# Kernel optimization log

Measured on AMD Instinct MI355X. Metric: run time of the kernel, lower is better.

Reference implementation:

```python
import jax, jax.numpy as jnp
import numpy as np

B, H, S, D = 2, 16, 2048, 128

def setup_inputs() -> dict:
    key = jax.random.key(0)
    kq, kk, kv = jax.random.split(key, 3)
    Q = jax.random.normal(kq, (B, H, S, D), dtype=jnp.float32)
    K = jax.random.normal(kk, (B, H, S, D), dtype=jnp.float32)
    V = jax.random.normal(kv, (B, H, S, D), dtype=jnp.float32)
    mask = jnp.tril(jnp.ones((S, S), dtype=bool))  # causal: 1 = keep
    return {"Q": Q, "K": K, "V": V, "mask": mask}

def reference(Q, K, V, mask):
    d_k = Q.shape[-1]
    scale = 1.0 / jnp.sqrt(jnp.asarray(d_k, dtype=Q.dtype))
    # [B,H,S,S] scores, matching the naive materialized implementation's math
    scores = jnp.einsum('bhqd,bhkd->bhqk', Q, K) * scale
    scores = jnp.where(mask, scores, jnp.asarray(-1e9, dtype=scores.dtype))
    attn = jax.nn.softmax(scores, axis=-1)
    return jnp.einsum('bhqk,bhkd->bhqd', attn, V)
```

## Files before the change

kernel.cpp:

```cpp
#include <hip/hip_runtime.h>
#include <hip/hip_bf16.h>
#include <stdint.h>

typedef __attribute__((ext_vector_type(8)))  __bf16 bf16x8;
typedef __attribute__((ext_vector_type(16))) float  f32x16;

#define B_  2
#define H_  16
#define S_  2048
#define D_  128
#define BH_ (B_*H_)

__device__ __forceinline__ uint32_t f2bf1(float f){
  uint32_t u = __builtin_bit_cast(uint32_t, f);
  return (u + 0x7fffu + ((u >> 16) & 1u)) >> 16;
}
__device__ __forceinline__ uint32_t pk2(float a, float b){
  return f2bf1(a) | (f2bf1(b) << 16);
}
__device__ __forceinline__ float bf2f(unsigned short u){
  return __builtin_bit_cast(float, (uint32_t)u << 16);
}

__device__ __forceinline__ void gld16(const void* g, void* l){
  __builtin_amdgcn_global_load_lds(
      (const __attribute__((address_space(1))) void*)g,
      (__attribute__((address_space(3))) void*)(uintptr_t)l, 16, 0, 0);
}

__device__ const unsigned char SPLIT_TAB[24] = {
  15*4+1,15*4+2, 7*4+0, 14*4+1,14*4+2, 13*4+1,13*4+2, 6*4+0,
  12*4+1,12*4+2, 11*4+1,11*4+2, 5*4+0, 10*4+1,10*4+2, 9*4+1,9*4+2,
  4*4+0, 8*4+1,8*4+2, 3*4+0, 2*4+0, 1*4+0, 0*4+0
};

__global__ void prep(const float* __restrict__ K, const float* __restrict__ V,
                     unsigned short* __restrict__ Kb, unsigned short* __restrict__ Vt){
  __shared__ __attribute__((aligned(16))) unsigned short t[64*68];
  const int kv0 = blockIdx.x * 64, d0 = blockIdx.y * 64, bh = blockIdx.z;
  const int tid = threadIdx.x;
  const float* Vp = V + (size_t)bh * S_ * D_;
  const float* Kp = K + (size_t)bh * S_ * D_;
  unsigned short* Ko = Kb + (size_t)bh * S_ * D_;
  for (int i = 0; i < 4; i++){
    int f = tid + i*256;
    int kv = f >> 4, c4 = f & 15;
    size_t idx = (size_t)(kv0+kv)*D_ + d0 + c4*4;
    float4 k = *(const float4*)(Kp + idx);
    *(uint2*)(Ko + idx) = make_uint2(pk2(k.x,k.y), pk2(k.z,k.w));
  }
  for (int i = 0; i < 4; i++){
    int f = tid + i*256;
    int kv = f >> 4, c4 = f & 15;
    float4 v = *(const float4*)(Vp + (size_t)(kv0+kv)*D_ + d0 + c4*4);
    *(uint2*)&t[kv*68 + c4*4] = make_uint2(pk2(v.x,v.y), pk2(v.z,v.w));
  }
  __syncthreads();
  unsigned short* Vo = Vt + (size_t)bh * D_ * S_;
  for (int i = 0; i < 4; i++){
    int g = tid + i*256;
    int d = g >> 4, c = g & 15, kv = c*4;
    ushort4 o;
    o.x = t[(kv+0)*68 + d];
    o.y = t[(kv+1)*68 + d];
    o.z = t[(kv+2)*68 + d];
    o.w = t[(kv+3)*68 + d];
    *(ushort4*)(Vo + (size_t)(d0+d)*S_ + kv0 + kv) = o;
  }
}

__global__ __launch_bounds__(256, 2)
void attn_fwd(const float* __restrict__ Q, const unsigned short* __restrict__ Kb,
              const unsigned short* __restrict__ Vt, float* __restrict__ Out,
              unsigned short* __restrict__ Opart, float* __restrict__ MLpart,
              int splitFlag){
  __shared__ __attribute__((aligned(16))) unsigned short Klds[2][64*128];
  __shared__ __attribute__((aligned(16))) unsigned short Vlds[2][128*64];

  const int bi = blockIdx.x;
  const int bh = (bi & 7) + 8*((bi >> 3) & 3);
  const int u  = bi >> 5;
  int qb, mode;
  if (splitFlag){ int c = SPLIT_TAB[u]; qb = c >> 2; mode = c & 3; }
  else { qb = (u < 8) ? (15 - u) : (u - 8); mode = 0; }

  const int tid  = threadIdx.x;
  const int wave = tid >> 6, lane = tid & 63;
  const int q32  = lane & 31, hf = lane >> 5;
  const int wq0  = qb*128 + wave*32;
  const int t0   = (mode == 2) ? qb + 1 : 0;
  const int tEnd = (mode == 1) ? qb + 1 : 2*qb + 2;
  const int dtw  = (mode == 1) ? (1 << 30) : (2*qb + (wave >> 1));
  const float qs = 0.08838834764831845f * 1.44269504088896f;

  const char* Kg = (const char*)(Kb + (size_t)bh * S_ * D_);
  const char* Vg = (const char*)(Vt + (size_t)bh * D_ * S_);

  uint32_t koff[4], voff[4];
  #pragma unroll
  for (int i = 0; i < 4; i++){
    int kr = wave*16 + i*4 + (lane >> 4);
    koff[i] = kr*256 + (((lane & 15) ^ (i*4 + (lane >> 4))) << 4);
    int vr = wave*32 + i*8 + (lane >> 3);
    voff[i] = vr*(S_*2) + (((lane & 7) ^ ((lane >> 3) & 7)) << 4);
  }

  auto stage = [&](int buf, int t){
    const char* kp = Kg + t*16384;
    const char* vp = Vg + t*128;
    char* kd = (char*)&Klds[buf][0] + wave*4096;
    char* vd = (char*)&Vlds[buf][0] + wave*4096;
    #pragma unroll
    for (int i = 0; i < 4; i++){
      gld16(kp + koff[i], kd + i*1024);
      gld16(vp + voff[i], vd + i*1024);
    }
  };

  uint4 qf[8];
  {
    const float* Qp = Q + ((size_t)bh * S_ + (wq0 + q32)) * D_ + hf*8;
    #pragma unroll
    for (int ds = 0; ds < 8; ds++){
      float4 a = *(const float4*)(Qp + ds*16);
      float4 b = *(const float4*)(Qp + ds*16 + 4);
      bf16x8 q8;
      q8[0] = (__bf16)(a.x*qs); q8[1] = (__bf16)(a.y*qs);
      q8[2] = (__bf16)(a.z*qs); q8[3] = (__bf16)(a.w*qs);
      q8[4] = (__bf16)(b.x*qs); q8[5] = (__bf16)(b.y*qs);
      q8[6] = (__bf16)(b.z*qs); q8[7] = (__bf16)(b.w*qs);
      qf[ds] = __builtin_bit_cast(uint4, q8);
    }
  }

  f32x16 o[4];
  #pragma unroll
  for (int db = 0; db < 4; db++) o[db] = (f32x16)(0.f);
  float m_run = -INFINITY, l_run = 0.f;

  stage(0, t0);
  __syncthreads();

  int cur = 0;
  for (int t = t0; t < tEnd; ++t){
    if (t + 1 < tEnd) stage(cur ^ 1, t + 1);

    if (t <= dtw){
      const bool diag = (t == dtw);
      const char* Kc = (const char*)&Klds[cur][0];
      const char* Vc = (const char*)&Vlds[cur][0];

      f32x16 sa0 = (f32x16)(0.f), sa1 = (f32x16)(0.f);
      __builtin_amdgcn_s_setprio(1);
      #pragma unroll
      for (int ds = 0; ds < 8; ds++){
        int c0 = (q32*256        + ds*32 + hf*16) ^ ((q32 & 15) << 4);
        int c1 = ((32+q32)*256   + ds*32 + hf*16) ^ ((q32 & 15) << 4);
        bf16x8 k0 = *(const bf16x8*)(Kc + c0);
        bf16x8 k1 = *(const bf16x8*)(Kc + c1);
        sa0 = __builtin_amdgcn_mfma_f32_32x32x16_bf16(
                k0, __builtin_bit_cast(bf16x8, qf[ds]), sa0, 0, 0, 0);
        sa1 = __builtin_amdgcn_mfma_f32_32x32x16_bf16(
                k1, __builtin_bit_cast(bf16x8, qf[ds]), sa1, 0, 0, 0);
      }
      __builtin_amdgcn_s_setprio(0);

      float p[32];
      float pm = -INFINITY;
      const int q_abs = wq0 + q32;
      #pragma unroll
      for (int r = 0; r < 16; r++){
        float s0 = sa0[r], s1 = sa1[r];
        if (diag){
          int kvl = t*64 + (r & 3) + 8*(r >> 2) + 4*hf;
          if (kvl      > q_abs) s0 = -1e30f;
          if (kvl + 32 > q_abs) s1 = -1e30f;
        }
        p[r] = s0; p[16 + r] = s1;
        pm = fmaxf(pm, fmaxf(s0, s1));
      }
      pm = fmaxf(pm, __shfl_xor(pm, 32));
      if (__any(pm > m_run + 11.5f)){
        float mn  = fmaxf(m_run, pm);
        float fac = exp2f(m_run - mn);
        float fv[16];
        #pragma unroll
        for (int r = 0; r < 16; r++) fv[r] = __shfl(fac, (r & 3) + 8*(r >> 2) + 4*hf);
        #pragma unroll
        for (int db = 0; db < 4; db++)
          #pragma unroll
          for (int r = 0; r < 16; r++) o[db][r] *= fv[r];
        l_run *= fac;
        m_run = mn;
      }
      float rs = 0.f;
      #pragma unroll
      for (int i = 0; i < 32; i++){ p[i] = exp2f(p[i] - m_run); rs += p[i]; }
      rs += __shfl_xor(rs, 32);
      l_run += rs;

      uint32_t W[8][2];
      #pragma unroll
      for (int M = 0; M < 8; M++){
        #pragma unroll
        for (int tt = 0; tt < 2; tt++){
          float lo = p[(M >> 2)*16 + 4*(M & 3) + 2*tt];
          float hi = p[(M >> 2)*16 + 4*(M & 3) + 2*tt + 1];
          asm("v_cvt_pk_bf16_f32 %0, %1, %2" : "=v"(W[M][tt]) : "v"(lo), "v"(hi));
        }
      }

      __builtin_amdgcn_s_setprio(1);
      #pragma unroll
      for (int Ks = 0; Ks < 4; Ks++){
        uint32_t d0 = W[2*Ks][0], d2 = W[2*Ks + 1][0];
        asm volatile("v_permlane32_swap_b32 %0, %1" : "+v"(d0), "+v"(d2));
        uint32_t d1 = W[2*Ks][1], d3 = W[2*Ks + 1][1];
        asm volatile("v_permlane32_swap_b32 %0, %1" : "+v"(d1), "+v"(d3));
        uint4 pw = make_uint4(d0, d1, d2, d3);
        bf16x8 paf = __builtin_bit_cast(bf16x8, pw);
        #pragma unroll
        for (int db = 0; db < 4; db++){
          int row = db*32 + q32;
          int vb = (row*128 + Ks*32 + hf*16) ^ ((row & 7) << 4);
          bf16x8 vf = *(const bf16x8*)(Vc + vb);
          o[db] = __builtin_amdgcn_mfma_f32_32x32x16_bf16(paf, vf, o[db], 0, 0, 0);
        }
      }
      __builtin_amdgcn_s_setprio(0);
    }

    __syncthreads();
    cur ^= 1;
  }

  if (mode == 0){
    float rl[16];
    #pragma unroll
    for (int r = 0; r < 16; r++)
      rl[r] = 1.f / __shfl(l_run, (r & 3) + 8*(r >> 2) + 4*hf);
    float* Op = Out + ((size_t)bh * S_ + wq0) * D_;
    #pragma unroll
    for (int db = 0; db < 4; db++){
      #pragma unroll
      for (int r = 0; r < 16; r++){
        int qrow = (r & 3) + 8*(r >> 2) + 4*hf;
        Op[(size_t)qrow*D_ + db*32 + q32] = o[db][r] * rl[r];
      }
    }
  } else {
    const int slot = (bh*8 + (qb - 8))*2 + (mode - 1);
    unsigned short* Po = Opart + (size_t)slot * (128*128);
    float* Ml = MLpart + (size_t)slot * 256;
    #pragma unroll
    for (int db = 0; db < 4; db++){
      #pragma unroll
      for (int r = 0; r < 16; r++){
        int row = wave*32 + (r & 3) + 8*(r >> 2) + 4*hf;
        __bf16 bv = (__bf16)o[db][r];
        Po[row*128 + db*32 + q32] = __builtin_bit_cast(unsigned short, bv);
      }
    }
    if (hf == 0){
      Ml[(wave*32 + q32)*2 + 0] = m_run;
      Ml[(wave*32 + q32)*2 + 1] = l_run;
    }
  }
}

__global__ __launch_bounds__(256)
void combine(const unsigned short* __restrict__ Opart,
             const float* __restrict__ MLpart, float* __restrict__ Out){
  const int blk = blockIdx.x;
  const int bh = blk >> 3, qq = blk & 7;
  const unsigned short* A  = Opart + (size_t)(blk*2) * (128*128);
  const unsigned short* Bp = A + 128*128;
  const float* MA = MLpart + (size_t)(blk*2) * 256;
  const float* MB = MA + 256;

  const int row  = threadIdx.x >> 1;
  const int half = threadIdx.x & 1;
  float mA = MA[row*2], lA = MA[row*2 + 1];
  float mB = MB[row*2], lB = MB[row*2 + 1];
  float M  = fmaxf(mA, mB);
  float wA = exp2f(mA - M), wB = exp2f(mB - M);
  float inv = 1.f / (lA*wA + lB*wB);
  wA *= inv; wB *= inv;

  const unsigned short* Ar = A  + row*128 + half*64;
  const unsigned short* Br = Bp + row*128 + half*64;
  float* Or = Out + ((size_t)bh * S_ + (qq + 8)*128 + row) * D_ + half*64;
  #pragma unroll
  for (int c = 0; c < 64; c += 8){
    ushort4 a0 = *(const ushort4*)(Ar + c), a1 = *(const ushort4*)(Ar + c + 4);
    ushort4 b0 = *(const ushort4*)(Br + c), b1 = *(const ushort4*)(Br + c + 4);
    const unsigned short av[8] = {a0.x,a0.y,a0.z,a0.w,a1.x,a1.y,a1.z,a1.w};
    const unsigned short bv[8] = {b0.x,b0.y,b0.z,b0.w,b1.x,b1.y,b1.z,b1.w};
    #pragma unroll
    for (int j = 0; j < 8; j++){
      Or[c + j] = bf2f(av[j])*wA + bf2f(bv[j])*wB;
    }
  }
}

extern "C" void kernel_launch(void* const* d_in, const int* in_sizes, int n_in,
                              void* d_out, int out_size, void* d_ws, size_t ws_size,
                              hipStream_t stream){
  const float* Q = (const float*)d_in[0];
  const float* K = (const float*)d_in[1];
  const float* V = (const float*)d_in[2];
  float* Out = (float*)d_out;

  unsigned short* Kb = (unsigned short*)d_ws;
  unsigned short* Vt = Kb + (size_t)BH_ * S_ * D_;
  unsigned short* Opart = Vt + (size_t)BH_ * S_ * D_;
  float* MLpart = (float*)(Opart + (size_t)512 * 128 * 128);

  const size_t need = (size_t)BH_*S_*D_*2*3 + (size_t)512*256*4;
  const int split = (ws_size >= need) ? 1 : 0;

  prep<<<dim3(S_/64, D_/64, BH_), 256, 0, stream>>>(K, V, Kb, Vt);
  attn_fwd<<<split ? 768 : 512, 256, 0, stream>>>(Q, Kb, Vt, Out, Opart, MLpart, split);
  if (split) combine<<<256, 256, 0, stream>>>(Opart, MLpart, Out);
}
```

Baseline: 101.6 us.

## Shrink KV tile to 32 and split long query blocks into up to four chunks

```diff
diff --git a/kernel.cpp b/kernel.cpp
--- a/kernel.cpp
+++ b/kernel.cpp
@@ -28,11 +28,17 @@
       (__attribute__((address_space(3))) void*)(uintptr_t)l, 16, 0, 0);
 }
 
-__device__ const unsigned char SPLIT_TAB[24] = {
-  15*4+1,15*4+2, 7*4+0, 14*4+1,14*4+2, 13*4+1,13*4+2, 6*4+0,
-  12*4+1,12*4+2, 11*4+1,11*4+2, 5*4+0, 10*4+1,10*4+2, 9*4+1,9*4+2,
-  4*4+0, 8*4+1,8*4+2, 3*4+0, 2*4+0, 1*4+0, 0*4+0
+__device__ const unsigned char TAB_S[40] = {
+  60,61,62,63, 44,45,46, 28,29, 12,
+  56,57,58,59, 40,41,
+  52,53,54,55, 42, 36, 24,25,
+  48,49,50,51, 37,38,
+  32,33,34, 20,21, 8,
+  16,17,
+  4,
+  0
 };
+__device__ const unsigned char OFFT[12] = {0,2,4,6,8,11,14,17,20,24,28,32};
 
 __global__ void prep(const float* __restrict__ K, const float* __restrict__ V,
                      unsigned short* __restrict__ Kb, unsigned short* __restrict__ Vt){
@@ -69,49 +75,58 @@
   }
 }
 
-__global__ __launch_bounds__(256, 2)
+__global__ __launch_bounds__(256, 4)
 void attn_fwd(const float* __restrict__ Q, const unsigned short* __restrict__ Kb,
               const unsigned short* __restrict__ Vt, float* __restrict__ Out,
               unsigned short* __restrict__ Opart, float* __restrict__ MLpart,
               int splitFlag){
-  __shared__ __attribute__((aligned(16))) unsigned short Klds[2][64*128];
-  __shared__ __attribute__((aligned(16))) unsigned short Vlds[2][128*64];
-
-  const int bi = blockIdx.x;
-  const int bh = (bi & 7) + 8*((bi >> 3) & 3);
-  const int u  = bi >> 5;
-  int qb, mode;
-  if (splitFlag){ int c = SPLIT_TAB[u]; qb = c >> 2; mode = c & 3; }
-  else { qb = (u < 8) ? (15 - u) : (u - 8); mode = 0; }
+  __shared__ __attribute__((aligned(16))) unsigned short Klds[2][32*128];
+  __shared__ __attribute__((aligned(16))) unsigned short Vlds[2][128*32];
+
+  const int bi  = blockIdx.x;
+  const int xcd = bi & 7;
+  const int idx = bi >> 3;
+  const int bh  = xcd + 8*(idx & 3);
+  const int ui  = idx >> 2;
+  int qb, c;
+  if (splitFlag){ int e = TAB_S[ui]; qb = e >> 2; c = e & 3; }
+  else { qb = 15 - ui; c = 0; }
+  const int nc = splitFlag ? ((qb >> 2) + 1) : 1;
+  const int nt = 4*qb + 4;
+  int t0, tEnd;
+  if (nc == 1){ t0 = 0; tEnd = nt; }
+  else {
+    int sz = nt/nc, rem = nt%nc;
+    t0 = c*sz + (c < rem ? c : rem);
+    tEnd = t0 + sz + (c < rem ? 1 : 0);
+  }
 
   const int tid  = threadIdx.x;
   const int wave = tid >> 6, lane = tid & 63;
   const int q32  = lane & 31, hf = lane >> 5;
   const int wq0  = qb*128 + wave*32;
-  const int t0   = (mode == 2) ? qb + 1 : 0;
-  const int tEnd = (mode == 1) ? qb + 1 : 2*qb + 2;
-  const int dtw  = (mode == 1) ? (1 << 30) : (2*qb + (wave >> 1));
+  const int dtw  = 4*qb + wave;
   const float qs = 0.08838834764831845f * 1.44269504088896f;
 
   const char* Kg = (const char*)(Kb + (size_t)bh * S_ * D_);
   const char* Vg = (const char*)(Vt + (size_t)bh * D_ * S_);
 
-  uint32_t koff[4], voff[4];
-  #pragma unroll
-  for (int i = 0; i < 4; i++){
-    int kr = wave*16 + i*4 + (lane >> 4);
-    koff[i] = kr*256 + (((lane & 15) ^ (i*4 + (lane >> 4))) << 4);
-    int vr = wave*32 + i*8 + (lane >> 3);
-    voff[i] = vr*(S_*2) + (((lane & 7) ^ ((lane >> 3) & 7)) << 4);
+  uint32_t koff[2], voff[2];
+  #pragma unroll
+  for (int i = 0; i < 2; i++){
+    int kr = wave*8 + i*4 + (lane >> 4);
+    koff[i] = kr*256 + (((lane & 15) ^ (kr & 15)) << 4);
+    int vr = wave*32 + i*16 + (lane >> 2);
+    voff[i] = vr*(S_*2) + (((lane & 3) ^ ((vr >> 1) & 3)) << 4);
   }
 
   auto stage = [&](int buf, int t){
-    const char* kp = Kg + t*16384;
-    const char* vp = Vg + t*128;
-    char* kd = (char*)&Klds[buf][0] + wave*4096;
-    char* vd = (char*)&Vlds[buf][0] + wave*4096;
-    #pragma unroll
-    for (int i = 0; i < 4; i++){
+    const char* kp = Kg + t*8192;
+    const char* vp = Vg + t*64;
+    char* kd = (char*)&Klds[buf][0] + wave*2048;
+    char* vd = (char*)&Vlds[buf][0] + wave*2048;
+    #pragma unroll
+    for (int i = 0; i < 2; i++){
       gld16(kp + koff[i], kd + i*1024);
       gld16(vp + voff[i], vd + i*1024);
     }
@@ -150,34 +165,29 @@
       const char* Kc = (const char*)&Klds[cur][0];
       const char* Vc = (const char*)&Vlds[cur][0];
 
-      f32x16 sa0 = (f32x16)(0.f), sa1 = (f32x16)(0.f);
+      f32x16 sa = (f32x16)(0.f);
       __builtin_amdgcn_s_setprio(1);
       #pragma unroll
       for (int ds = 0; ds < 8; ds++){
-        int c0 = (q32*256        + ds*32 + hf*16) ^ ((q32 & 15) << 4);
-        int c1 = ((32+q32)*256   + ds*32 + hf*16) ^ ((q32 & 15) << 4);
-        bf16x8 k0 = *(const bf16x8*)(Kc + c0);
-        bf16x8 k1 = *(const bf16x8*)(Kc + c1);
-        sa0 = __builtin_amdgcn_mfma_f32_32x32x16_bf16(
-                k0, __builtin_bit_cast(bf16x8, qf[ds]), sa0, 0, 0, 0);
-        sa1 = __builtin_amdgcn_mfma_f32_32x32x16_bf16(
-                k1, __builtin_bit_cast(bf16x8, qf[ds]), sa1, 0, 0, 0);
+        int cb = (q32*256 + ds*32 + hf*16) ^ ((q32 & 15) << 4);
+        bf16x8 kf = *(const bf16x8*)(Kc + cb);
+        sa = __builtin_amdgcn_mfma_f32_32x32x16_bf16(
+               kf, __builtin_bit_cast(bf16x8, qf[ds]), sa, 0, 0, 0);
       }
       __builtin_amdgcn_s_setprio(0);
 
-      float p[32];
+      float p[16];
       float pm = -INFINITY;
       const int q_abs = wq0 + q32;
       #pragma unroll
       for (int r = 0; r < 16; r++){
-        float s0 = sa0[r], s1 = sa1[r];
+        float s = sa[r];
         if (diag){
-          int kvl = t*64 + (r & 3) + 8*(r >> 2) + 4*hf;
-          if (kvl      > q_abs) s0 = -1e30f;
-          if (kvl + 32 > q_abs) s1 = -1e30f;
+          int kvl = t*32 + (r & 3) + 8*(r >> 2) + 4*hf;
+          if (kvl > q_abs) s = -1e30f;
         }
-        p[r] = s0; p[16 + r] = s1;
-        pm = fmaxf(pm, fmaxf(s0, s1));
+        p[r] = s;
+        pm = fmaxf(pm, s);
       }
       pm = fmaxf(pm, __shfl_xor(pm, 32));
       if (__any(pm > m_run + 11.5f)){
@@ -195,34 +205,34 @@
       }
       float rs = 0.f;
       #pragma unroll
-      for (int i = 0; i < 32; i++){ p[i] = exp2f(p[i] - m_run); rs += p[i]; }
+      for (int i = 0; i < 16; i++){ p[i] = exp2f(p[i] - m_run); rs += p[i]; }
       rs += __shfl_xor(rs, 32);
       l_run += rs;
 
-      uint32_t W[8][2];
-      #pragma unroll
-      for (int M = 0; M < 8; M++){
+      uint32_t Wp[4][2];
+      #pragma unroll
+      for (int m = 0; m < 4; m++){
         #pragma unroll
         for (int tt = 0; tt < 2; tt++){
-          float lo = p[(M >> 2)*16 + 4*(M & 3) + 2*tt];
-          float hi = p[(M >> 2)*16 + 4*(M & 3) + 2*tt + 1];
-          asm("v_cvt_pk_bf16_f32 %0, %1, %2" : "=v"(W[M][tt]) : "v"(lo), "v"(hi));
+          float lo = p[4*m + 2*tt];
+          float hi = p[4*m + 2*tt + 1];
+          asm("v_cvt_pk_bf16_f32 %0, %1, %2" : "=v"(Wp[m][tt]) : "v"(lo), "v"(hi));
         }
       }
 
       __builtin_amdgcn_s_setprio(1);
       #pragma unroll
-      for (int Ks = 0; Ks < 4; Ks++){
-        uint32_t d0 = W[2*Ks][0], d2 = W[2*Ks + 1][0];
+      for (int Ks = 0; Ks < 2; Ks++){
+        uint32_t d0 = Wp[2*Ks][0], d2 = Wp[2*Ks + 1][0];
         asm volatile("v_permlane32_swap_b32 %0, %1" : "+v"(d0), "+v"(d2));
-        uint32_t d1 = W[2*Ks][1], d3 = W[2*Ks + 1][1];
+        uint32_t d1 = Wp[2*Ks][1], d3 = Wp[2*Ks + 1][1];
         asm volatile("v_permlane32_swap_b32 %0, %1" : "+v"(d1), "+v"(d3));
         uint4 pw = make_uint4(d0, d1, d2, d3);
         bf16x8 paf = __builtin_bit_cast(bf16x8, pw);
         #pragma unroll
         for (int db = 0; db < 4; db++){
           int row = db*32 + q32;
-          int vb = (row*128 + Ks*32 + hf*16) ^ ((row & 7) << 4);
+          int vb = (row*64 + Ks*32 + hf*16) ^ (((row >> 1) & 3) << 4);
           bf16x8 vf = *(const bf16x8*)(Vc + vb);
           o[db] = __builtin_amdgcn_mfma_f32_32x32x16_bf16(paf, vf, o[db], 0, 0, 0);
         }
@@ -234,7 +244,7 @@
     cur ^= 1;
   }
 
-  if (mode == 0){
+  if (nc == 1){
     float rl[16];
     #pragma unroll
     for (int r = 0; r < 16; r++)
@@ -249,7 +259,7 @@
       }
     }
   } else {
-    const int slot = (bh*8 + (qb - 8))*2 + (mode - 1);
+    const int slot = bh*36 + OFFT[qb - 4] + c;
     unsigned short* Po = Opart + (size_t)slot * (128*128);
     float* Ml = MLpart + (size_t)slot * 256;
     #pragma unroll
@@ -271,35 +281,46 @@
 __global__ __launch_bounds__(256)
 void combine(const unsigned short* __restrict__ Opart,
              const float* __restrict__ MLpart, float* __restrict__ Out){
-  const int blk = blockIdx.x;
-  const int bh = blk >> 3, qq = blk & 7;
-  const unsigned short* A  = Opart + (size_t)(blk*2) * (128*128);
-  const unsigned short* Bp = A + 128*128;
-  const float* MA = MLpart + (size_t)(blk*2) * 256;
-  const float* MB = MA + 256;
-
+  const int bx = blockIdx.x;
+  const int bh = bx / 12, qi = bx % 12, qb = qi + 4;
+  const int nc = (qb >> 2) + 1;
+  const int base = bh*36 + OFFT[qi];
   const int row  = threadIdx.x >> 1;
   const int half = threadIdx.x & 1;
-  float mA = MA[row*2], lA = MA[row*2 + 1];
-  float mB = MB[row*2], lB = MB[row*2 + 1];
-  float M  = fmaxf(mA, mB);
-  float wA = exp2f(mA - M), wB = exp2f(mB - M);
-  float inv = 1.f / (lA*wA + lB*wB);
-  wA *= inv; wB *= inv;
-
-  const unsigned short* Ar = A  + row*128 + half*64;
-  const unsigned short* Br = Bp + row*128 + half*64;
-  float* Or = Out + ((size_t)bh * S_ + (qq + 8)*128 + row) * D_ + half*64;
-  #pragma unroll
-  for (int c = 0; c < 64; c += 8){
-    ushort4 a0 = *(const ushort4*)(Ar + c), a1 = *(const ushort4*)(Ar + c + 4);
-    ushort4 b0 = *(const ushort4*)(Br + c), b1 = *(const ushort4*)(Br + c + 4);
-    const unsigned short av[8] = {a0.x,a0.y,a0.z,a0.w,a1.x,a1.y,a1.z,a1.w};
-    const unsigned short bv[8] = {b0.x,b0.y,b0.z,b0.w,b1.x,b1.y,b1.z,b1.w};
-    #pragma unroll
-    for (int j = 0; j < 8; j++){
-      Or[c + j] = bf2f(av[j])*wA + bf2f(bv[j])*wB;
-    }
+
+  float m[4] = {-INFINITY,-INFINITY,-INFINITY,-INFINITY};
+  float l[4] = {0.f,0.f,0.f,0.f};
+  float M = -INFINITY;
+  #pragma unroll
+  for (int c = 0; c < 4; c++) if (c < nc){
+    m[c] = MLpart[(size_t)(base+c)*256 + row*2];
+    l[c] = MLpart[(size_t)(base+c)*256 + row*2 + 1];
+    M = fmaxf(M, m[c]);
+  }
+  float w[4] = {0.f,0.f,0.f,0.f};
+  float den = 0.f;
+  #pragma unroll
+  for (int c = 0; c < 4; c++) if (c < nc){
+    w[c] = exp2f(m[c] - M);
+    den += l[c]*w[c];
+  }
+  float inv = 1.f / den;
+
+  float* Or = Out + ((size_t)bh * S_ + qb*128 + row) * D_ + half*64;
+  #pragma unroll
+  for (int cc = 0; cc < 64; cc += 8){
+    float acc[8] = {0,0,0,0,0,0,0,0};
+    #pragma unroll
+    for (int c = 0; c < 4; c++) if (c < nc){
+      const unsigned short* Pr = Opart + (size_t)(base+c)*16384 + row*128 + half*64 + cc;
+      ushort4 a0 = *(const ushort4*)(Pr), a1 = *(const ushort4*)(Pr + 4);
+      acc[0] += bf2f(a0.x)*w[c]; acc[1] += bf2f(a0.y)*w[c];
+      acc[2] += bf2f(a0.z)*w[c]; acc[3] += bf2f(a0.w)*w[c];
+      acc[4] += bf2f(a1.x)*w[c]; acc[5] += bf2f(a1.y)*w[c];
+      acc[6] += bf2f(a1.z)*w[c]; acc[7] += bf2f(a1.w)*w[c];
+    }
+    #pragma unroll
+    for (int j = 0; j < 8; j++) Or[cc + j] = acc[j]*inv;
   }
 }
 
@@ -314,12 +335,13 @@
   unsigned short* Kb = (unsigned short*)d_ws;
   unsigned short* Vt = Kb + (size_t)BH_ * S_ * D_;
   unsigned short* Opart = Vt + (size_t)BH_ * S_ * D_;
-  float* MLpart = (float*)(Opart + (size_t)512 * 128 * 128);
-
-  const size_t need = (size_t)BH_*S_*D_*2*3 + (size_t)512*256*4;
+  float* MLpart = (float*)(Opart + (size_t)1152 * 128 * 128);
+
+  const size_t need = (size_t)BH_*S_*D_*2*2
+                    + (size_t)1152*128*128*2 + (size_t)1152*256*4;
   const int split = (ws_size >= need) ? 1 : 0;
 
   prep<<<dim3(S_/64, D_/64, BH_), 256, 0, stream>>>(K, V, Kb, Vt);
-  attn_fwd<<<split ? 768 : 512, 256, 0, stream>>>(Q, Kb, Vt, Out, Opart, MLpart, split);
-  if (split) combine<<<256, 256, 0, stream>>>(Opart, MLpart, Out);
-}
+  attn_fwd<<<split ? 1280 : 512, 256, 0, stream>>>(Q, Kb, Vt, Out, Opart, MLpart, split);
+  if (split) combine<<<384, 256, 0, stream>>>(Opart, MLpart, Out);
+}
```

Measured after the change: 225.1 us. +121.5%, slower.

## Use 32-wide KV tiles with triple-buffered LDS and software-pipelined QK

Applied to the files above, without the earlier changes.

```diff
diff --git a/kernel.cpp b/kernel.cpp
--- a/kernel.cpp
+++ b/kernel.cpp
@@ -69,13 +69,12 @@
   }
 }
 
-__global__ __launch_bounds__(256, 2)
+__global__ __launch_bounds__(256, 3)
 void attn_fwd(const float* __restrict__ Q, const unsigned short* __restrict__ Kb,
               const unsigned short* __restrict__ Vt, float* __restrict__ Out,
               unsigned short* __restrict__ Opart, float* __restrict__ MLpart,
               int splitFlag){
-  __shared__ __attribute__((aligned(16))) unsigned short Klds[2][64*128];
-  __shared__ __attribute__((aligned(16))) unsigned short Vlds[2][128*64];
+  __shared__ __attribute__((aligned(16))) char Sh[3*16384];
 
   const int bi = blockIdx.x;
   const int bh = (bi & 7) + 8*((bi >> 3) & 3);
@@ -88,30 +87,31 @@
   const int wave = tid >> 6, lane = tid & 63;
   const int q32  = lane & 31, hf = lane >> 5;
   const int wq0  = qb*128 + wave*32;
-  const int t0   = (mode == 2) ? qb + 1 : 0;
-  const int tEnd = (mode == 1) ? qb + 1 : 2*qb + 2;
-  const int dtw  = (mode == 1) ? (1 << 30) : (2*qb + (wave >> 1));
+  const int t0   = (mode == 2) ? 2*qb + 2 : 0;
+  const int tEnd = (mode == 1) ? 2*qb + 2 : 4*qb + 4;
+  const int dtw  = (mode == 1) ? (1 << 30) : (4*qb + wave);
   const float qs = 0.08838834764831845f * 1.44269504088896f;
 
   const char* Kg = (const char*)(Kb + (size_t)bh * S_ * D_);
   const char* Vg = (const char*)(Vt + (size_t)bh * D_ * S_);
 
-  uint32_t koff[4], voff[4];
+  uint32_t koff[2], voff[2];
   #pragma unroll
-  for (int i = 0; i < 4; i++){
-    int kr = wave*16 + i*4 + (lane >> 4);
-    koff[i] = kr*256 + (((lane & 15) ^ (i*4 + (lane >> 4))) << 4);
-    int vr = wave*32 + i*8 + (lane >> 3);
-    voff[i] = vr*(S_*2) + (((lane & 7) ^ ((lane >> 3) & 7)) << 4);
+  for (int i = 0; i < 2; i++){
+    int kr = wave*8 + i*4 + (lane >> 4);
+    koff[i] = kr*256 + (((lane & 15) ^ (kr & 15)) << 4);
+    int vr = wave*32 + i*16 + (lane >> 2);
+    voff[i] = vr*(S_*2) + (((lane & 3) ^ ((vr >> 1) & 3)) << 4);
   }
 
   auto stage = [&](int buf, int t){
-    const char* kp = Kg + t*16384;
-    const char* vp = Vg + t*128;
-    char* kd = (char*)&Klds[buf][0] + wave*4096;
-    char* vd = (char*)&Vlds[buf][0] + wave*4096;
-    #pragma unroll
-    for (int i = 0; i < 4; i++){
+    const char* kp = Kg + t*8192;
+    const char* vp = Vg + t*64;
+    char* base = Sh + buf*16384;
+    char* kd = base + wave*2048;
+    char* vd = base + 8192 + wave*2048;
+    #pragma unroll
+    for (int i = 0; i < 2; i++){
       gld16(kp + koff[i], kd + i*1024);
       gld16(vp + voff[i], vd + i*1024);
     }
@@ -138,46 +138,50 @@
   for (int db = 0; db < 4; db++) o[db] = (f32x16)(0.f);
   float m_run = -INFINITY, l_run = 0.f;
 
-  stage(0, t0);
-  __syncthreads();
-
-  int cur = 0;
+  auto qk = [&](int buf){
+    const char* Kc = Sh + buf*16384;
+    f32x16 s = (f32x16)(0.f);
+    __builtin_amdgcn_s_setprio(1);
+    #pragma unroll
+    for (int ds = 0; ds < 8; ds++){
+      int cb = (q32*256 + ds*32 + hf*16) ^ ((q32 & 15) << 4);
+      bf16x8 kf = *(const bf16x8*)(Kc + cb);
+      s = __builtin_amdgcn_mfma_f32_32x32x16_bf16(
+            kf, __builtin_bit_cast(bf16x8, qf[ds]), s, 0, 0, 0);
+    }
+    __builtin_amdgcn_s_setprio(0);
+    return s;
+  };
+
+  stage(t0 % 3, t0);
+  if (t0 + 1 < tEnd) stage((t0 + 1) % 3, t0 + 1);
+  asm volatile("s_waitcnt vmcnt(0)" ::: "memory");
+  __builtin_amdgcn_s_barrier();
+  __builtin_amdgcn_sched_barrier(0);
+
+  f32x16 sc = qk(t0 % 3);
+
   for (int t = t0; t < tEnd; ++t){
-    if (t + 1 < tEnd) stage(cur ^ 1, t + 1);
+    if (t + 2 < tEnd) stage((t + 2) % 3, t + 2);
+
+    f32x16 sn;
+    const bool nxt = (t + 1 < tEnd) && (t + 1 <= dtw);
+    if (nxt) sn = qk((t + 1) % 3);
 
     if (t <= dtw){
       const bool diag = (t == dtw);
-      const char* Kc = (const char*)&Klds[cur][0];
-      const char* Vc = (const char*)&Vlds[cur][0];
-
-      f32x16 sa0 = (f32x16)(0.f), sa1 = (f32x16)(0.f);
-      __builtin_amdgcn_s_setprio(1);
-      #pragma unroll
-      for (int ds = 0; ds < 8; ds++){
-        int c0 = (q32*256        + ds*32 + hf*16) ^ ((q32 & 15) << 4);
-        int c1 = ((32+q32)*256   + ds*32 + hf*16) ^ ((q32 & 15) << 4);
-        bf16x8 k0 = *(const bf16x8*)(Kc + c0);
-        bf16x8 k1 = *(const bf16x8*)(Kc + c1);
-        sa0 = __builtin_amdgcn_mfma_f32_32x32x16_bf16(
-                k0, __builtin_bit_cast(bf16x8, qf[ds]), sa0, 0, 0, 0);
-        sa1 = __builtin_amdgcn_mfma_f32_32x32x16_bf16(
-                k1, __builtin_bit_cast(bf16x8, qf[ds]), sa1, 0, 0, 0);
-      }
-      __builtin_amdgcn_s_setprio(0);
-
-      float p[32];
+      float p[16];
       float pm = -INFINITY;
       const int q_abs = wq0 + q32;
       #pragma unroll
       for (int r = 0; r < 16; r++){
-        float s0 = sa0[r], s1 = sa1[r];
+        float s = sc[r];
         if (diag){
-          int kvl = t*64 + (r & 3) + 8*(r >> 2) + 4*hf;
-          if (kvl      > q_abs) s0 = -1e30f;
-          if (kvl + 32 > q_abs) s1 = -1e30f;
+          int kvl = t*32 + (r & 3) + 8*(r >> 2) + 4*hf;
+          if (kvl > q_abs) s = -1e30f;
         }
-        p[r] = s0; p[16 + r] = s1;
-        pm = fmaxf(pm, fmaxf(s0, s1));
+        p[r] = s;
+        pm = fmaxf(pm, s);
       }
       pm = fmaxf(pm, __shfl_xor(pm, 32));
       if (__any(pm > m_run + 11.5f)){
@@ -195,34 +199,35 @@
       }
       float rs = 0.f;
       #pragma unroll
-      for (int i = 0; i < 32; i++){ p[i] = exp2f(p[i] - m_run); rs += p[i]; }
+      for (int i = 0; i < 16; i++){ p[i] = exp2f(p[i] - m_run); rs += p[i]; }
       rs += __shfl_xor(rs, 32);
       l_run += rs;
 
-      uint32_t W[8][2];
-      #pragma unroll
-      for (int M = 0; M < 8; M++){
+      uint32_t Wp[4][2];
+      #pragma unroll
+      for (int m = 0; m < 4; m++){
         #pragma unroll
         for (int tt = 0; tt < 2; tt++){
-          float lo = p[(M >> 2)*16 + 4*(M & 3) + 2*tt];
-          float hi = p[(M >> 2)*16 + 4*(M & 3) + 2*tt + 1];
-          asm("v_cvt_pk_bf16_f32 %0, %1, %2" : "=v"(W[M][tt]) : "v"(lo), "v"(hi));
+          float lo = p[4*m + 2*tt];
+          float hi = p[4*m + 2*tt + 1];
+          asm("v_cvt_pk_bf16_f32 %0, %1, %2" : "=v"(Wp[m][tt]) : "v"(lo), "v"(hi));
         }
       }
 
+      const char* Vc = Sh + (t % 3)*16384 + 8192;
       __builtin_amdgcn_s_setprio(1);
       #pragma unroll
-      for (int Ks = 0; Ks < 4; Ks++){
-        uint32_t d0 = W[2*Ks][0], d2 = W[2*Ks + 1][0];
+      for (int Ks = 0; Ks < 2; Ks++){
+        uint32_t d0 = Wp[2*Ks][0], d2 = Wp[2*Ks + 1][0];
         asm volatile("v_permlane32_swap_b32 %0, %1" : "+v"(d0), "+v"(d2));
-        uint32_t d1 = W[2*Ks][1], d3 = W[2*Ks + 1][1];
+        uint32_t d1 = Wp[2*Ks][1], d3 = Wp[2*Ks + 1][1];
         asm volatile("v_permlane32_swap_b32 %0, %1" : "+v"(d1), "+v"(d3));
         uint4 pw = make_uint4(d0, d1, d2, d3);
         bf16x8 paf = __builtin_bit_cast(bf16x8, pw);
         #pragma unroll
         for (int db = 0; db < 4; db++){
           int row = db*32 + q32;
-          int vb = (row*128 + Ks*32 + hf*16) ^ ((row & 7) << 4);
+          int vb = (row*64 + Ks*32 + hf*16) ^ (((row >> 1) & 3) << 4);
           bf16x8 vf = *(const bf16x8*)(Vc + vb);
           o[db] = __builtin_amdgcn_mfma_f32_32x32x16_bf16(paf, vf, o[db], 0, 0, 0);
         }
@@ -230,8 +235,10 @@
       __builtin_amdgcn_s_setprio(0);
     }
 
-    __syncthreads();
-    cur ^= 1;
+    asm volatile("s_waitcnt vmcnt(0)" ::: "memory");
+    __builtin_amdgcn_s_barrier();
+    __builtin_amdgcn_sched_barrier(0);
+    if (nxt) sc = sn;
   }
 
   if (mode == 0){
```

Result: slower. 128.9 us (+26.8%).
